# Kernel optimization log

Hardware: AMD Instinct MI355X
Metric: run time of the kernel (lower is better)

Reference implementation:

```python
import jax, jax.numpy as jnp
import numpy as np

NEG_SLOPE = 0.2  # PyG GATConv default leaky_relu slope


def _gat_layer(x, W, att_src, att_dst, bias, src, dst, num_nodes, heads, out_c, concat):
    # x: [N, F_in] -> h: [N, H, C]
    h = (x @ W).reshape(num_nodes, heads, out_c)
    a_src = jnp.einsum('nhc,hc->nh', h, att_src)  # [N, H]
    a_dst = jnp.einsum('nhc,hc->nh', h, att_dst)  # [N, H]
    # edge (src -> dst): attention logit per edge/head
    e = jax.nn.leaky_relu(a_src[src] + a_dst[dst], NEG_SLOPE)  # [E, H]
    # softmax over edges sharing the same destination node
    m = jax.ops.segment_max(e, dst, num_segments=num_nodes)  # [N, H]
    m = jnp.where(jnp.isfinite(m), m, 0.0)
    ex = jnp.exp(e - m[dst])
    denom = jax.ops.segment_sum(ex, dst, num_segments=num_nodes)  # [N, H]
    alpha = ex / (denom[dst] + 1e-16)  # [E, H]
    # weighted scatter-add aggregation
    msg = h[src] * alpha[:, :, None]  # [E, H, C]
    out = jax.ops.segment_sum(msg, dst, num_segments=num_nodes)  # [N, H, C]
    if concat:
        out = out.reshape(num_nodes, heads * out_c)
    else:
        out = out.mean(axis=1)
    return out + bias


def _add_self_loops(edge_index, num_nodes):
    loop = jnp.arange(num_nodes, dtype=edge_index.dtype)
    src = jnp.concatenate([edge_index[0], loop])
    dst = jnp.concatenate([edge_index[1], loop])
    return src, dst


def setup_inputs() -> dict:
    key = jax.random.key(0)
    ks = jax.random.split(key, 9)
    N, F_in, E, H, C, OUT = 30000, 256, 300000, 8, 128, 64
    x = jax.random.normal(ks[0], (N, F_in), dtype=jnp.float32)
    edge_index = jax.random.randint(ks[1], (2, E), 0, N, dtype=jnp.int32)
    s1 = 1.0 / np.sqrt(F_in)
    s2 = 1.0 / np.sqrt(H * C)
    return {
        'x': x,
        'edge_index': edge_index,
        'W1': jax.random.normal(ks[2], (F_in, H * C), dtype=jnp.float32) * s1,
        'att_src1': jax.random.normal(ks[3], (H, C), dtype=jnp.float32) * s2,
        'att_dst1': jax.random.normal(ks[4], (H, C), dtype=jnp.float32) * s2,
        'b1': jnp.zeros((H * C,), dtype=jnp.float32),
        'W2': jax.random.normal(ks[5], (H * C, OUT), dtype=jnp.float32) * s2,
        'att_src2': jax.random.normal(ks[6], (1, OUT), dtype=jnp.float32) * 0.125,
        'att_dst2': jax.random.normal(ks[7], (1, OUT), dtype=jnp.float32) * 0.125,
        'b2': jnp.zeros((OUT,), dtype=jnp.float32),
    }


def reference(x, edge_index, W1, att_src1, att_dst1, b1, W2, att_src2, att_dst2, b2):
    N = x.shape[0]
    src, dst = _add_self_loops(edge_index, N)
    # dropout layers are identity in eval mode
    h = _gat_layer(x, W1, att_src1, att_dst1, b1, src, dst, N, 8, 128, True)
    h = jax.nn.elu(h)
    out = _gat_layer(h, W2, att_src2, att_dst2, b2, src, dst, N, 1, 64, False)
    return jax.nn.log_softmax(out, axis=-1)
```

## Files before the change

### kernel.cpp

```cpp
#include <hip/hip_runtime.h>
#include <math.h>

#define N_NODES 30000
#define F_IN 256
#define E_RAW 300000
#define E_TOT (E_RAW + N_NODES)
#define HEADS 8
#define CH 128
#define HC 1024
#define OUTC 64
#define NEG_SLOPE 0.2f
#define CAP 64

typedef __attribute__((ext_vector_type(8))) short bf16x8;
typedef __attribute__((ext_vector_type(4))) float f32x4;
typedef __attribute__((ext_vector_type(2))) float f32x2;

__device__ __forceinline__ float bf2f(unsigned short u) {
    return __uint_as_float(((unsigned)u) << 16);
}
__device__ __forceinline__ unsigned short f2bf(float f) {
    unsigned b = __float_as_uint(f);
    b += 0x7FFFu + ((b >> 16) & 1u);
    return (unsigned short)(b >> 16);
}
__device__ __forceinline__ void edge_sd(const int* __restrict__ ei, int e, int& s, int& d) {
    if (e < E_RAW) { s = ei[e]; d = ei[E_RAW + e]; }
    else           { s = e - E_RAW; d = s; }
}
__device__ __forceinline__ void async_cp16(const void* g, void* l) {
    __builtin_amdgcn_global_load_lds((const __attribute__((address_space(1))) void*)g,
                                     (__attribute__((address_space(3))) void*)l, 16, 0, 0);
}
__device__ __forceinline__ int slotP(int s) {
    return ((s >> 6) << 6) + ((s >> 2) & 15) + ((s & 3) << 4);
}
__device__ __forceinline__ void wave_sync() {
    __builtin_amdgcn_fence(__ATOMIC_ACQ_REL, "wavefront");
    __builtin_amdgcn_wave_barrier();
}

#define NB_CVTX (N_NODES * F_IN / 4 / 256)
#define NB_DEG  ((E_TOT + 255) / 256)
#define NB_W1T  ((F_IN * HC + 255) / 256)
#define NB_W2T  ((HC * OUTC + 255) / 256)
#define NB_PREP (NB_CVTX + NB_DEG + NB_W1T + NB_W2T)

__global__ __launch_bounds__(256)
void prep_kernel(const float* __restrict__ x, unsigned short* __restrict__ xb,
                 const float* __restrict__ W1, unsigned short* __restrict__ W1t,
                 const float* __restrict__ W2, unsigned short* __restrict__ W2t,
                 const int* __restrict__ ei, int* __restrict__ deg)
{
    const int b = blockIdx.x, t = threadIdx.x;
    if (b < NB_CVTX) {
        int i = b * 256 + t;
        const float4 v = reinterpret_cast<const float4*>(x)[i];
        ushort4 o;
        o.x = f2bf(v.x); o.y = f2bf(v.y); o.z = f2bf(v.z); o.w = f2bf(v.w);
        reinterpret_cast<ushort4*>(xb)[i] = o;
    } else if (b < NB_CVTX + NB_DEG) {
        int e = (b - NB_CVTX) * 256 + t;
        if (e < E_TOT) {
            int s, d; edge_sd(ei, e, s, d);
            atomicAdd(&deg[d], 1);
        }
    } else if (b < NB_CVTX + NB_DEG + NB_W1T) {
        int i = (b - NB_CVTX - NB_DEG) * 256 + t;
        if (i < F_IN * HC) {
            int k = i >> 10, n = i & (HC - 1);
            W1t[n * F_IN + k] = f2bf(W1[i]);
        }
    } else {
        int i = (b - NB_CVTX - NB_DEG - NB_W1T) * 256 + t;
        if (i < HC * OUTC) {
            int s = i >> 6, n = i & (OUTC - 1);
            W2t[n * HC + s] = f2bf(W2[slotP(s) * OUTC + n]);
        }
    }
}

__global__ __launch_bounds__(256)
void gemm1_mfma(const unsigned short* __restrict__ A,
                const unsigned short* __restrict__ Bt,
                unsigned* __restrict__ Cp,
                const float* __restrict__ att_src, const float* __restrict__ att_dst,
                float* __restrict__ a_src, float* __restrict__ a_dst, int M)
{
    __shared__ unsigned short Al[128 * 64];
    __shared__ unsigned short Bl[128 * 64];
    __shared__ float s_src[128][2];
    __shared__ float s_dst[128][2];
    const int tid  = threadIdx.x;
    const int wave = tid >> 6, lane = tid & 63;
    const int quad = lane >> 4, l16 = lane & 15;
    const int wr = (wave >> 1) * 64, wc = (wave & 1) * 64;
    const int row0 = blockIdx.y * 128;
    const int col0 = blockIdx.x * 128;

    f32x4 acc[4][4];
#pragma unroll
    for (int i = 0; i < 4; i++)
#pragma unroll
        for (int j = 0; j < 4; j++) acc[i][j] = (f32x4){0.f, 0.f, 0.f, 0.f};

    for (int k0 = 0; k0 < F_IN; k0 += 64) {
#pragma unroll
        for (int p = 0; p < 4; p++) {
            int idx = tid + 256 * p;
            int r = idx >> 3, q = idx & 7;
            async_cp16(A + (size_t)(row0 + r) * F_IN + k0 + ((q ^ (r & 7)) * 8),
                       Al + (size_t)(wave * 64 + 256 * p) * 8);
        }
#pragma unroll
        for (int p = 0; p < 4; p++) {
            int idx = tid + 256 * p;
            int r = idx >> 3, q = idx & 7;
            async_cp16(Bt + (size_t)(col0 + r) * F_IN + k0 + ((q ^ (r & 7)) * 8),
                       Bl + (size_t)(wave * 64 + 256 * p) * 8);
        }
        __syncthreads();
#pragma unroll
        for (int kh = 0; kh < 2; kh++) {
            const int cx = (kh * 4 + quad) ^ (l16 & 7);
            bf16x8 af[4], bg[4];
#pragma unroll
            for (int i = 0; i < 4; i++)
                af[i] = *reinterpret_cast<const bf16x8*>(Al + ((wr + i * 16 + l16) * 8 + cx) * 8);
#pragma unroll
            for (int j = 0; j < 4; j++)
                bg[j] = *reinterpret_cast<const bf16x8*>(Bl + ((wc + j * 16 + l16) * 8 + cx) * 8);
#pragma unroll
            for (int i = 0; i < 4; i++)
#pragma unroll
                for (int j = 0; j < 4; j++)
                    acc[i][j] = __builtin_amdgcn_mfma_f32_16x16x32_bf16(af[i], bg[j], acc[i][j], 0, 0, 0);
        }
        __syncthreads();
    }
    const int D = ((col0 + wc) >> 6) * 16 + l16;
#pragma unroll
    for (int i = 0; i < 4; i++) {
#pragma unroll
        for (int r = 0; r < 4; r++) {
            int row = row0 + wr + i * 16 + quad * 4 + r;
            if (row >= M) continue;
            int w8 = __builtin_amdgcn_cvt_pk_fp8_f32(acc[i][0][r], acc[i][1][r], 0, false);
            w8 = __builtin_amdgcn_cvt_pk_fp8_f32(acc[i][2][r], acc[i][3][r], w8, true);
            Cp[(size_t)row * 256 + D] = (unsigned)w8;
        }
    }
    const float* asv = att_src + blockIdx.x * CH;
    const float* adv = att_dst + blockIdx.x * CH;
    float av[4], dv[4];
#pragma unroll
    for (int j = 0; j < 4; j++) {
        av[j] = asv[wc + j * 16 + l16];
        dv[j] = adv[wc + j * 16 + l16];
    }
#pragma unroll
    for (int i = 0; i < 4; i++) {
#pragma unroll
        for (int r = 0; r < 4; r++) {
            float ps = 0.f, pd = 0.f;
#pragma unroll
            for (int j = 0; j < 4; j++) {
                float cc = acc[i][j][r];
                ps += cc * av[j];
                pd += cc * dv[j];
            }
#pragma unroll
            for (int o = 1; o < 16; o <<= 1) {
                ps += __shfl_xor(ps, o);
                pd += __shfl_xor(pd, o);
            }
            if (l16 == 0) {
                int lr = wr + i * 16 + quad * 4 + r;
                s_src[lr][wc >> 6] = ps;
                s_dst[lr][wc >> 6] = pd;
            }
        }
    }
    __syncthreads();
    if (tid < 128) {
        int row = row0 + tid;
        if (row < M) {
            a_src[row * 8 + blockIdx.x] = s_src[tid][0] + s_src[tid][1];
            a_dst[row * 8 + blockIdx.x] = s_dst[tid][0] + s_dst[tid][1];
        }
    }
}

__global__ __launch_bounds__(256)
void gemm2_mfma(const unsigned short* __restrict__ A,
                const unsigned short* __restrict__ Bt,
                unsigned short* __restrict__ C,
                const float* __restrict__ att_src2, const float* __restrict__ att_dst2,
                float* __restrict__ a_src2, float* __restrict__ a_dst2, int M)
{
    __shared__ unsigned short Al[64 * 64];
    __shared__ unsigned short Bl[64 * 64];
    const int tid  = threadIdx.x;
    const int wave = tid >> 6, lane = tid & 63;
    const int quad = lane >> 4, l16 = lane & 15;
    const int wr = wave * 16;
    const int row0 = blockIdx.x * 64;

    f32x4 acc[4];
#pragma unroll
    for (int j = 0; j < 4; j++) acc[j] = (f32x4){0.f, 0.f, 0.f, 0.f};

    for (int k0 = 0; k0 < HC; k0 += 64) {
#pragma unroll
        for (int p = 0; p < 2; p++) {
            int idx = tid + 256 * p;
            int r = idx >> 3, q = idx & 7;
            async_cp16(A + (size_t)(row0 + r) * HC + k0 + ((q ^ (r & 7)) * 8),
                       Al + (size_t)(wave * 64 + 256 * p) * 8);
        }
#pragma unroll
        for (int p = 0; p < 2; p++) {
            int idx = tid + 256 * p;
            int r = idx >> 3, q = idx & 7;
            async_cp16(Bt + (size_t)r * HC + k0 + ((q ^ (r & 7)) * 8),
                       Bl + (size_t)(wave * 64 + 256 * p) * 8);
        }
        __syncthreads();
#pragma unroll
        for (int kh = 0; kh < 2; kh++) {
            const int cx = (kh * 4 + quad) ^ (l16 & 7);
            bf16x8 af, bg[4];
            af = *reinterpret_cast<const bf16x8*>(Al + ((wr + l16) * 8 + cx) * 8);
#pragma unroll
            for (int j = 0; j < 4; j++)
                bg[j] = *reinterpret_cast<const bf16x8*>(Bl + ((j * 16 + l16) * 8 + cx) * 8);
#pragma unroll
            for (int j = 0; j < 4; j++)
                acc[j] = __builtin_amdgcn_mfma_f32_16x16x32_bf16(af, bg[j], acc[j], 0, 0, 0);
        }
        __syncthreads();
    }
    float av[4], dv[4];
#pragma unroll
    for (int j = 0; j < 4; j++) {
        av[j] = att_src2[j * 16 + l16];
        dv[j] = att_dst2[j * 16 + l16];
    }
#pragma unroll
    for (int r = 0; r < 4; r++) {
        int row = row0 + wr + quad * 4 + r;
        float ps = 0.f, pd = 0.f;
#pragma unroll
        for (int j = 0; j < 4; j++) {
            float cc = acc[j][r];
            int col = j * 16 + l16;
            if (row < M) C[(size_t)row * OUTC + col] = f2bf(cc);
            ps += cc * av[j];
            pd += cc * dv[j];
        }
#pragma unroll
        for (int o = 1; o < 16; o <<= 1) {
            ps += __shfl_xor(ps, o);
            pd += __shfl_xor(pd, o);
        }
        if (l16 == 0 && row < M) {
            a_src2[row] = ps;
            a_dst2[row] = pd;
        }
    }
}

__global__ __launch_bounds__(256)
void alloc_kernel(const int* __restrict__ deg, int* __restrict__ rowstart,
                  int* __restrict__ cursor, int* __restrict__ counter)
{
    int d = blockIdx.x * 256 + threadIdx.x;
    int lane = threadIdx.x & 63;
    int v = (d < N_NODES) ? deg[d] : 0;
    int x = v;
#pragma unroll
    for (int o = 1; o < 64; o <<= 1) {
        int y = __shfl_up(x, o);
        if (lane >= o) x += y;
    }
    int excl = x - v;
    int total = __shfl(x, 63);
    int base = 0;
    if (lane == 63) base = atomicAdd(counter, total);
    base = __shfl(base, 63);
    if (d < N_NODES) {
        rowstart[d] = base + excl;
        cursor[d]   = base + excl;
    }
}

__global__ void scatter_kernel(const int* __restrict__ ei, int* __restrict__ cursor,
                               int* __restrict__ csr_src)
{
    int e = blockIdx.x * 256 + threadIdx.x;
    if (e >= E_TOT) return;
    int s, d; edge_sd(ei, e, s, d);
    int pos = atomicAdd(&cursor[d], 1);
    csr_src[pos] = s;
}

__global__ __launch_bounds__(256)
void agg1_fused(const int* __restrict__ rowstart, const int* __restrict__ degv,
                const int* __restrict__ csr_src,
                const unsigned* __restrict__ h1p,
                const float* __restrict__ a_src1, const float* __restrict__ a_dst1,
                const float* __restrict__ b1, unsigned short* __restrict__ out1)
{
    const int t   = threadIdx.x;
    const int sub = t >> 6;
    const int tl  = t & 63;
    const int h   = tl >> 3;
    const int d   = blockIdx.x * 4 + sub;

    __shared__ float exps[4][CAP * 8];
    __shared__ int   srcs[4][CAP];

    const int start = rowstart[d];
    const int deg   = degv[d];

    const float adst = a_dst1[d * 8 + h];
    const uint4* __restrict__ h1v = reinterpret_cast<const uint4*>(h1p);

    float denom_part = 0.f;
    float acc[16];
#pragma unroll
    for (int k = 0; k < 16; k++) acc[k] = 0.f;

    for (int c0 = 0; c0 < deg; c0 += CAP) {
        const int cend = min(deg - c0, CAP);
        for (int c = (tl & 7); c < cend; c += 8) {
            int s = csr_src[start + c0 + c];
            if (h == 0) srcs[sub][c] = s;
            float a = a_src1[s * 8 + h] + adst;
            float v = a > 0.f ? a : NEG_SLOPE * a;
            float ex = __expf(v);
            exps[sub][c * 8 + h] = ex;
            denom_part += ex;
        }
        wave_sync();
        {
            int   s_cur = srcs[sub][0];
            float w_cur = exps[sub][h];
            uint4 u_cur = h1v[(size_t)s_cur * 64 + tl];
            for (int c = 0; c < cend; c++) {
                int   s_nxt = 0; float w_nxt = 0.f; uint4 u_nxt;
                if (c + 1 < cend) {
                    s_nxt = srcs[sub][c + 1];
                    w_nxt = exps[sub][(c + 1) * 8 + h];
                    u_nxt = h1v[(size_t)s_nxt * 64 + tl];
                }
#pragma unroll
                for (int dw = 0; dw < 4; dw++) {
                    unsigned wd = (&u_cur.x)[dw];
                    f32x2 lo = __builtin_amdgcn_cvt_pk_f32_fp8((int)wd, false);
                    f32x2 hi = __builtin_amdgcn_cvt_pk_f32_fp8((int)wd, true);
                    acc[dw * 4 + 0] += w_cur * lo.x;
                    acc[dw * 4 + 1] += w_cur * lo.y;
                    acc[dw * 4 + 2] += w_cur * hi.x;
                    acc[dw * 4 + 3] += w_cur * hi.y;
                }
                s_cur = s_nxt; w_cur = w_nxt; u_cur = u_nxt;
            }
        }
        wave_sync();
    }
#pragma unroll
    for (int o = 1; o < 8; o <<= 1) denom_part += __shfl_xor(denom_part, o);
    const float dinv = 1.f / (denom_part + 1e-16f);

    unsigned short ov[16];
#pragma unroll
    for (int e = 0; e < 16; e++) {
        float v = acc[e] * dinv + b1[slotP(16 * tl + e)];
        v = v > 0.f ? v : __expf(v) - 1.f;
        ov[e] = f2bf(v);
    }
    uint4* op = reinterpret_cast<uint4*>(out1 + (size_t)d * HC + 16 * tl);
    op[0] = *reinterpret_cast<uint4*>(&ov[0]);
    op[1] = *reinterpret_cast<uint4*>(&ov[8]);
}

__global__ __launch_bounds__(256)
void agg2_lsm(const int* __restrict__ rowstart, const int* __restrict__ degv,
              const int* __restrict__ csr_src,
              const unsigned short* __restrict__ h2,
              const float* __restrict__ a_src2, const float* __restrict__ a_dst2,
              const float* __restrict__ b2, float* __restrict__ out)
{
    const int t = threadIdx.x;
    const int sub  = t >> 6;
    const int lane = t & 63;
    const int eo   = lane >> 4;
    const int cq   = lane & 15;
    const int d = blockIdx.x * 4 + sub;

    __shared__ float exs[4][CAP];
    __shared__ int   ss[4][CAP];

    const int start = rowstart[d];
    const int deg   = degv[d];

    const float adst = a_dst2[d];
    const uint2* __restrict__ h2v = reinterpret_cast<const uint2*>(h2);
    float denom_part = 0.f;
    float ax = 0.f, ay = 0.f, az = 0.f, aw = 0.f;

    for (int c0 = 0; c0 < deg; c0 += CAP) {
        const int cend = min(deg - c0, CAP);
        for (int c = lane; c < cend; c += 64) {
            int s = csr_src[start + c0 + c];
            ss[sub][c] = s;
            float a = a_src2[s] + adst;
            float v = a > 0.f ? a : NEG_SLOPE * a;
            float ex = __expf(v);
            exs[sub][c] = ex;
            denom_part += ex;
        }
        wave_sync();
        {
            int   cc = eo;
            float w0 = (cc < cend) ? exs[sub][cc] : 0.f;
            int   s0 = (cc < cend) ? ss[sub][cc] : ss[sub][0];
            uint2 u0 = h2v[(size_t)s0 * 16 + cq];
            for (int c = 0; c + 4 < cend; c += 4) {
                int cc1 = c + 4 + eo;
                float w1 = (cc1 < cend) ? exs[sub][cc1] : 0.f;
                int   s1 = (cc1 < cend) ? ss[sub][cc1] : ss[sub][0];
                uint2 u1 = h2v[(size_t)s1 * 16 + cq];
                ax += w0 * __uint_as_float(u0.x << 16);
                ay += w0 * __uint_as_float(u0.x & 0xFFFF0000u);
                az += w0 * __uint_as_float(u0.y << 16);
                aw += w0 * __uint_as_float(u0.y & 0xFFFF0000u);
                w0 = w1; s0 = s1; u0 = u1;
            }
            ax += w0 * __uint_as_float(u0.x << 16);
            ay += w0 * __uint_as_float(u0.x & 0xFFFF0000u);
            az += w0 * __uint_as_float(u0.y << 16);
            aw += w0 * __uint_as_float(u0.y & 0xFFFF0000u);
        }
        wave_sync();
    }
    ax += __shfl_xor(ax, 16); ax += __shfl_xor(ax, 32);
    ay += __shfl_xor(ay, 16); ay += __shfl_xor(ay, 32);
    az += __shfl_xor(az, 16); az += __shfl_xor(az, 32);
    aw += __shfl_xor(aw, 16); aw += __shfl_xor(aw, 32);
#pragma unroll
    for (int o = 32; o > 0; o >>= 1) denom_part += __shfl_xor(denom_part, o);
    const float dinv = 1.f / (denom_part + 1e-16f);

    float4 bb = reinterpret_cast<const float4*>(b2)[cq];
    float v0 = ax * dinv + bb.x;
    float v1 = ay * dinv + bb.y;
    float v2 = az * dinv + bb.z;
    float v3 = aw * dinv + bb.w;
    float m = fmaxf(fmaxf(v0, v1), fmaxf(v2, v3));
#pragma unroll
    for (int o = 1; o < 16; o <<= 1) m = fmaxf(m, __shfl_xor(m, o));
    float ex = __expf(v0 - m) + __expf(v1 - m) + __expf(v2 - m) + __expf(v3 - m);
    float ssum = ex;
#pragma unroll
    for (int o = 1; o < 16; o <<= 1) ssum += __shfl_xor(ssum, o);
    if (eo == 0) {
        float lg = __logf(ssum);
        reinterpret_cast<float4*>(out + (size_t)d * OUTC)[cq] =
            make_float4(v0 - m - lg, v1 - m - lg, v2 - m - lg, v3 - m - lg);
    }
}

extern "C" void kernel_launch(void* const* d_in, const int* in_sizes, int n_in,
                              void* d_out, int out_size, void* d_ws, size_t ws_size,
                              hipStream_t stream)
{
    const float* x   = (const float*)d_in[0];
    const int*   ei  = (const int*)d_in[1];
    const float* W1  = (const float*)d_in[2];
    const float* as1 = (const float*)d_in[3];
    const float* ad1 = (const float*)d_in[4];
    const float* b1  = (const float*)d_in[5];
    const float* W2  = (const float*)d_in[6];
    const float* as2 = (const float*)d_in[7];
    const float* ad2 = (const float*)d_in[8];
    const float* b2  = (const float*)d_in[9];

    char* p = (char*)d_ws;
    auto alloc = [&](size_t bytes) { char* r = p; p += (bytes + 255) & ~(size_t)255; return r; };

    char* region0 = (char*)alloc((size_t)N_NODES * HC * 2);
    unsigned* h1p = (unsigned*)region0;

    char* region1 = (char*)alloc((size_t)N_NODES * HC * 2);
    unsigned short* out1 = (unsigned short*)region1;
    unsigned short* xb   = (unsigned short*)region1;
    unsigned short* W1t  = (unsigned short*)(region1 + (size_t)N_NODES * F_IN * 2 + 256);

    unsigned short* W2t = (unsigned short*)alloc((size_t)OUTC * HC * 2);

    float* a_src1   = (float*)alloc((size_t)N_NODES * HEADS * 4);
    float* a_dst1   = (float*)alloc((size_t)N_NODES * HEADS * 4);
    int*   deg      = (int*)alloc((size_t)(N_NODES + 1) * 4);
    int*   counter  = deg + N_NODES;
    int*   rowstart = (int*)alloc((size_t)N_NODES * 4);
    int*   cursor   = (int*)alloc((size_t)N_NODES * 4);
    int*   csr_src  = (int*)alloc((size_t)E_TOT * 4);

    char* q = region0;
    auto alias = [&](size_t bytes) { char* r = q; q += (bytes + 255) & ~(size_t)255; return r; };
    unsigned short* h2 = (unsigned short*)alias((size_t)N_NODES * OUTC * 2);
    float* a_src2  = (float*)alias((size_t)N_NODES * 4);
    float* a_dst2  = (float*)alias((size_t)N_NODES * 4);

    hipMemsetAsync(deg, 0, (size_t)(N_NODES + 1) * 4, stream);

    prep_kernel<<<NB_PREP, 256, 0, stream>>>(x, xb, W1, W1t, W2, W2t, ei, deg);

    alloc_kernel<<<(N_NODES + 255) / 256, 256, 0, stream>>>(deg, rowstart, cursor, counter);
    scatter_kernel<<<(E_TOT + 255) / 256, 256, 0, stream>>>(ei, cursor, csr_src);

    gemm1_mfma<<<dim3(HC / 128, (N_NODES + 127) / 128), 256, 0, stream>>>(
        xb, W1t, h1p, as1, ad1, a_src1, a_dst1, N_NODES);
    agg1_fused<<<N_NODES / 4, 256, 0, stream>>>(rowstart, deg, csr_src, h1p, a_src1, a_dst1, b1, out1);

    gemm2_mfma<<<(N_NODES + 63) / 64, 256, 0, stream>>>(
        out1, W2t, h2, as2, ad2, a_src2, a_dst2, N_NODES);
    agg2_lsm<<<N_NODES / 4, 256, 0, stream>>>(rowstart, deg, csr_src, h2, a_src2, a_dst2, b2, (float*)d_out);
}
```

Measured before the change: 259.0 us.

## Precompute attention logits via folded W1·att vectors and per-edge exp weights in scatter

Folds att_src/att_dst into W1 (x·(W1·att)) so layer-1 attention logits are computed in fp32 from x during the prep pass, instead of in the GEMM epilogue. The scatter kernel then computes the per-edge exp2 weights (log2e pre-scaled, no max subtraction) and stores them in CSR order, so agg1 no longer gathers a_src or computes exponentials. agg1 also gets a two-deep prefetch and packed FMA accumulation. The costs are an extra small kernel, a 10.5MB per-edge weight buffer, and dropping the softmax max-shift, which assumes the logits stay small.

```diff
diff --git a/kernel.cpp b/kernel.cpp
--- a/kernel.cpp
+++ b/kernel.cpp
@@ -11,14 +11,12 @@
 #define OUTC 64
 #define NEG_SLOPE 0.2f
 #define CAP 64
+#define LOG2E 1.44269504f
 
 typedef __attribute__((ext_vector_type(8))) short bf16x8;
 typedef __attribute__((ext_vector_type(4))) float f32x4;
 typedef __attribute__((ext_vector_type(2))) float f32x2;
 
-__device__ __forceinline__ float bf2f(unsigned short u) {
-    return __uint_as_float(((unsigned)u) << 16);
-}
 __device__ __forceinline__ unsigned short f2bf(float f) {
     unsigned b = __float_as_uint(f);
     b += 0x7FFFu + ((b >> 16) & 1u);
@@ -39,8 +37,32 @@
     __builtin_amdgcn_fence(__ATOMIC_ACQ_REL, "wavefront");
     __builtin_amdgcn_wave_barrier();
 }
-
-#define NB_CVTX (N_NODES * F_IN / 4 / 256)
+__device__ __forceinline__ f32x2 pk_fma(f32x2 a, f32x2 b, f32x2 c) {
+    f32x2 d;
+    asm("v_pk_fma_f32 %0, %1, %2, %3" : "=v"(d) : "v"(a), "v"(b), "v"(c));
+    return d;
+}
+__device__ __forceinline__ float wexp(float t) {
+    return __builtin_amdgcn_exp2f(fmaxf(t, NEG_SLOPE * t));
+}
+
+__global__ __launch_bounds__(256)
+void vsrc_kernel(const float* __restrict__ W1, const float* __restrict__ att_src,
+                 const float* __restrict__ att_dst, float* __restrict__ vsd)
+{
+    const int j = blockIdx.x;
+    const int k = threadIdx.x;
+    const int hj = j & 7;
+    const float* av = (j < 8 ? att_src : att_dst) + hj * CH;
+    const float* wr = W1 + (size_t)k * HC + hj * CH;
+    float s = 0.f;
+#pragma unroll 4
+    for (int c = 0; c < CH; c += 4)
+        s += wr[c] * av[c] + wr[c + 1] * av[c + 1] + wr[c + 2] * av[c + 2] + wr[c + 3] * av[c + 3];
+    vsd[j * 256 + k] = s;
+}
+
+#define NB_CVTX (N_NODES / 16)
 #define NB_DEG  ((E_TOT + 255) / 256)
 #define NB_W1T  ((F_IN * HC + 255) / 256)
 #define NB_W2T  ((HC * OUTC + 255) / 256)
@@ -50,15 +72,40 @@
 void prep_kernel(const float* __restrict__ x, unsigned short* __restrict__ xb,
                  const float* __restrict__ W1, unsigned short* __restrict__ W1t,
                  const float* __restrict__ W2, unsigned short* __restrict__ W2t,
-                 const int* __restrict__ ei, int* __restrict__ deg)
+                 const int* __restrict__ ei, int* __restrict__ deg,
+                 const float* __restrict__ vsd,
+                 float* __restrict__ a_src1, float* __restrict__ a_dst1)
 {
     const int b = blockIdx.x, t = threadIdx.x;
     if (b < NB_CVTX) {
-        int i = b * 256 + t;
-        const float4 v = reinterpret_cast<const float4*>(x)[i];
-        ushort4 o;
-        o.x = f2bf(v.x); o.y = f2bf(v.y); o.z = f2bf(v.z); o.w = f2bf(v.w);
-        reinterpret_cast<ushort4*>(xb)[i] = o;
+        const int w = t >> 6, l = t & 63;
+        const int n0 = b * 16 + w * 4;
+        float4 vs[16];
+        const float4* vs4 = reinterpret_cast<const float4*>(vsd);
+#pragma unroll
+        for (int j = 0; j < 16; j++) vs[j] = vs4[j * 64 + l];
+#pragma unroll 1
+        for (int nn = 0; nn < 4; nn++) {
+            const int n = n0 + nn;
+            const float4 v = reinterpret_cast<const float4*>(x)[(size_t)n * 64 + l];
+            ushort4 o;
+            o.x = f2bf(v.x); o.y = f2bf(v.y); o.z = f2bf(v.z); o.w = f2bf(v.w);
+            reinterpret_cast<ushort4*>(xb)[(size_t)n * 64 + l] = o;
+            float pp[16];
+#pragma unroll
+            for (int j = 0; j < 16; j++)
+                pp[j] = v.x * vs[j].x + v.y * vs[j].y + v.z * vs[j].z + v.w * vs[j].w;
+#pragma unroll
+            for (int o2 = 1; o2 < 64; o2 <<= 1)
+#pragma unroll
+                for (int j = 0; j < 16; j++) pp[j] += __shfl_xor(pp[j], o2);
+            float sel = pp[0];
+#pragma unroll
+            for (int j = 1; j < 16; j++) if (l == j) sel = pp[j];
+            sel *= LOG2E;
+            if (l < 8)       a_src1[n * 8 + l] = sel;
+            else if (l < 16) a_dst1[n * 8 + (l - 8)] = sel;
+        }
     } else if (b < NB_CVTX + NB_DEG) {
         int e = (b - NB_CVTX) * 256 + t;
         if (e < E_TOT) {
@@ -76,196 +123,6 @@
         if (i < HC * OUTC) {
             int s = i >> 6, n = i & (OUTC - 1);
             W2t[n * HC + s] = f2bf(W2[slotP(s) * OUTC + n]);
-        }
-    }
-}
-
-__global__ __launch_bounds__(256)
-void gemm1_mfma(const unsigned short* __restrict__ A,
-                const unsigned short* __restrict__ Bt,
-                unsigned* __restrict__ Cp,
-                const float* __restrict__ att_src, const float* __restrict__ att_dst,
-                float* __restrict__ a_src, float* __restrict__ a_dst, int M)
-{
-    __shared__ unsigned short Al[128 * 64];
-    __shared__ unsigned short Bl[128 * 64];
-    __shared__ float s_src[128][2];
-    __shared__ float s_dst[128][2];
-    const int tid  = threadIdx.x;
-    const int wave = tid >> 6, lane = tid & 63;
-    const int quad = lane >> 4, l16 = lane & 15;
-    const int wr = (wave >> 1) * 64, wc = (wave & 1) * 64;
-    const int row0 = blockIdx.y * 128;
-    const int col0 = blockIdx.x * 128;
-
-    f32x4 acc[4][4];
-#pragma unroll
-    for (int i = 0; i < 4; i++)
-#pragma unroll
-        for (int j = 0; j < 4; j++) acc[i][j] = (f32x4){0.f, 0.f, 0.f, 0.f};
-
-    for (int k0 = 0; k0 < F_IN; k0 += 64) {
-#pragma unroll
-        for (int p = 0; p < 4; p++) {
-            int idx = tid + 256 * p;
-            int r = idx >> 3, q = idx & 7;
-            async_cp16(A + (size_t)(row0 + r) * F_IN + k0 + ((q ^ (r & 7)) * 8),
-                       Al + (size_t)(wave * 64 + 256 * p) * 8);
-        }
-#pragma unroll
-        for (int p = 0; p < 4; p++) {
-            int idx = tid + 256 * p;
-            int r = idx >> 3, q = idx & 7;
-            async_cp16(Bt + (size_t)(col0 + r) * F_IN + k0 + ((q ^ (r & 7)) * 8),
-                       Bl + (size_t)(wave * 64 + 256 * p) * 8);
-        }
-        __syncthreads();
-#pragma unroll
-        for (int kh = 0; kh < 2; kh++) {
-            const int cx = (kh * 4 + quad) ^ (l16 & 7);
-            bf16x8 af[4], bg[4];
-#pragma unroll
-            for (int i = 0; i < 4; i++)
-                af[i] = *reinterpret_cast<const bf16x8*>(Al + ((wr + i * 16 + l16) * 8 + cx) * 8);
-#pragma unroll
-            for (int j = 0; j < 4; j++)
-                bg[j] = *reinterpret_cast<const bf16x8*>(Bl + ((wc + j * 16 + l16) * 8 + cx) * 8);
-#pragma unroll
-            for (int i = 0; i < 4; i++)
-#pragma unroll
-                for (int j = 0; j < 4; j++)
-                    acc[i][j] = __builtin_amdgcn_mfma_f32_16x16x32_bf16(af[i], bg[j], acc[i][j], 0, 0, 0);
-        }
-        __syncthreads();
-    }
-    const int D = ((col0 + wc) >> 6) * 16 + l16;
-#pragma unroll
-    for (int i = 0; i < 4; i++) {
-#pragma unroll
-        for (int r = 0; r < 4; r++) {
-            int row = row0 + wr + i * 16 + quad * 4 + r;
-            if (row >= M) continue;
-            int w8 = __builtin_amdgcn_cvt_pk_fp8_f32(acc[i][0][r], acc[i][1][r], 0, false);
-            w8 = __builtin_amdgcn_cvt_pk_fp8_f32(acc[i][2][r], acc[i][3][r], w8, true);
-            Cp[(size_t)row * 256 + D] = (unsigned)w8;
-        }
-    }
-    const float* asv = att_src + blockIdx.x * CH;
-    const float* adv = att_dst + blockIdx.x * CH;
-    float av[4], dv[4];
-#pragma unroll
-    for (int j = 0; j < 4; j++) {
-        av[j] = asv[wc + j * 16 + l16];
-        dv[j] = adv[wc + j * 16 + l16];
-    }
-#pragma unroll
-    for (int i = 0; i < 4; i++) {
-#pragma unroll
-        for (int r = 0; r < 4; r++) {
-            float ps = 0.f, pd = 0.f;
-#pragma unroll
-            for (int j = 0; j < 4; j++) {
-                float cc = acc[i][j][r];
-                ps += cc * av[j];
-                pd += cc * dv[j];
-            }
-#pragma unroll
-            for (int o = 1; o < 16; o <<= 1) {
-                ps += __shfl_xor(ps, o);
-                pd += __shfl_xor(pd, o);
-            }
-            if (l16 == 0) {
-                int lr = wr + i * 16 + quad * 4 + r;
-                s_src[lr][wc >> 6] = ps;
-                s_dst[lr][wc >> 6] = pd;
-            }
-        }
-    }
-    __syncthreads();
-    if (tid < 128) {
-        int row = row0 + tid;
-        if (row < M) {
-            a_src[row * 8 + blockIdx.x] = s_src[tid][0] + s_src[tid][1];
-            a_dst[row * 8 + blockIdx.x] = s_dst[tid][0] + s_dst[tid][1];
-        }
-    }
-}
-
-__global__ __launch_bounds__(256)
-void gemm2_mfma(const unsigned short* __restrict__ A,
-                const unsigned short* __restrict__ Bt,
-                unsigned short* __restrict__ C,
-                const float* __restrict__ att_src2, const float* __restrict__ att_dst2,
-                float* __restrict__ a_src2, float* __restrict__ a_dst2, int M)
-{
-    __shared__ unsigned short Al[64 * 64];
-    __shared__ unsigned short Bl[64 * 64];
-    const int tid  = threadIdx.x;
-    const int wave = tid >> 6, lane = tid & 63;
-    const int quad = lane >> 4, l16 = lane & 15;
-    const int wr = wave * 16;
-    const int row0 = blockIdx.x * 64;
-
-    f32x4 acc[4];
-#pragma unroll
-    for (int j = 0; j < 4; j++) acc[j] = (f32x4){0.f, 0.f, 0.f, 0.f};
-
-    for (int k0 = 0; k0 < HC; k0 += 64) {
-#pragma unroll
-        for (int p = 0; p < 2; p++) {
-            int idx = tid + 256 * p;
-            int r = idx >> 3, q = idx & 7;
-            async_cp16(A + (size_t)(row0 + r) * HC + k0 + ((q ^ (r & 7)) * 8),
-                       Al + (size_t)(wave * 64 + 256 * p) * 8);
-        }
-#pragma unroll
-        for (int p = 0; p < 2; p++) {
-            int idx = tid + 256 * p;
-            int r = idx >> 3, q = idx & 7;
-            async_cp16(Bt + (size_t)r * HC + k0 + ((q ^ (r & 7)) * 8),
-                       Bl + (size_t)(wave * 64 + 256 * p) * 8);
-        }
-        __syncthreads();
-#pragma unroll
-        for (int kh = 0; kh < 2; kh++) {
-            const int cx = (kh * 4 + quad) ^ (l16 & 7);
-            bf16x8 af, bg[4];
-            af = *reinterpret_cast<const bf16x8*>(Al + ((wr + l16) * 8 + cx) * 8);
-#pragma unroll
-            for (int j = 0; j < 4; j++)
-                bg[j] = *reinterpret_cast<const bf16x8*>(Bl + ((j * 16 + l16) * 8 + cx) * 8);
-#pragma unroll
-            for (int j = 0; j < 4; j++)
-                acc[j] = __builtin_amdgcn_mfma_f32_16x16x32_bf16(af, bg[j], acc[j], 0, 0, 0);
-        }
-        __syncthreads();
-    }
-    float av[4], dv[4];
-#pragma unroll
-    for (int j = 0; j < 4; j++) {
-        av[j] = att_src2[j * 16 + l16];
-        dv[j] = att_dst2[j * 16 + l16];
-    }
-#pragma unroll
-    for (int r = 0; r < 4; r++) {
-        int row = row0 + wr + quad * 4 + r;
-        float ps = 0.f, pd = 0.f;
-#pragma unroll
-        for (int j = 0; j < 4; j++) {
-            float cc = acc[j][r];
-            int col = j * 16 + l16;
-            if (row < M) C[(size_t)row * OUTC + col] = f2bf(cc);
-            ps += cc * av[j];
-            pd += cc * dv[j];
-        }
-#pragma unroll
-        for (int o = 1; o < 16; o <<= 1) {
-            ps += __shfl_xor(ps, o);
-            pd += __shfl_xor(pd, o);
-        }
-        if (l16 == 0 && row < M) {
-            a_src2[row] = ps;
-            a_dst2[row] = pd;
         }
     }
 }
@@ -295,26 +152,110 @@
 }
 
 __global__ void scatter_kernel(const int* __restrict__ ei, int* __restrict__ cursor,
-                               int* __restrict__ csr_src)
+                               int* __restrict__ csr_src,
+                               const float* __restrict__ a_src1,
+                               const float* __restrict__ a_dst1,
+                               float* __restrict__ wcsr)
 {
     int e = blockIdx.x * 256 + threadIdx.x;
     if (e >= E_TOT) return;
     int s, d; edge_sd(ei, e, s, d);
     int pos = atomicAdd(&cursor[d], 1);
     csr_src[pos] = s;
+    const float4* A4 = reinterpret_cast<const float4*>(a_src1);
+    const float4* D4 = reinterpret_cast<const float4*>(a_dst1);
+    float4 sa = A4[s * 2 + 0], sb = A4[s * 2 + 1];
+    float4 da = D4[d * 2 + 0], db = D4[d * 2 + 1];
+    float4 w0, w1;
+    w0.x = wexp(sa.x + da.x); w0.y = wexp(sa.y + da.y);
+    w0.z = wexp(sa.z + da.z); w0.w = wexp(sa.w + da.w);
+    w1.x = wexp(sb.x + db.x); w1.y = wexp(sb.y + db.y);
+    w1.z = wexp(sb.z + db.z); w1.w = wexp(sb.w + db.w);
+    reinterpret_cast<float4*>(wcsr)[pos * 2 + 0] = w0;
+    reinterpret_cast<float4*>(wcsr)[pos * 2 + 1] = w1;
+}
+
+__global__ __launch_bounds__(256)
+void gemm1_mfma(const unsigned short* __restrict__ A,
+                const unsigned short* __restrict__ Bt,
+                unsigned* __restrict__ Cp,
+                int M)
+{
+    __shared__ unsigned short Al[128 * 64];
+    __shared__ unsigned short Bl[128 * 64];
+    const int tid  = threadIdx.x;
+    const int wave = tid >> 6, lane = tid & 63;
+    const int quad = lane >> 4, l16 = lane & 15;
+    const int wr = (wave >> 1) * 64, wc = (wave & 1) * 64;
+    const int row0 = blockIdx.y * 128;
+    const int col0 = blockIdx.x * 128;
+
+    f32x4 acc[4][4];
+#pragma unroll
+    for (int i = 0; i < 4; i++)
+#pragma unroll
+        for (int j = 0; j < 4; j++) acc[i][j] = (f32x4){0.f, 0.f, 0.f, 0.f};
+
+    for (int k0 = 0; k0 < F_IN; k0 += 64) {
+#pragma unroll
+        for (int p = 0; p < 4; p++) {
+            int idx = tid + 256 * p;
+            int r = idx >> 3, q = idx & 7;
+            async_cp16(A + (size_t)(row0 + r) * F_IN + k0 + ((q ^ (r & 7)) * 8),
+                       Al + (size_t)(wave * 64 + 256 * p) * 8);
+        }
+#pragma unroll
+        for (int p = 0; p < 4; p++) {
+            int idx = tid + 256 * p;
+            int r = idx >> 3, q = idx & 7;
+            async_cp16(Bt + (size_t)(col0 + r) * F_IN + k0 + ((q ^ (r & 7)) * 8),
+                       Bl + (size_t)(wave * 64 + 256 * p) * 8);
+        }
+        __syncthreads();
+#pragma unroll
+        for (int kh = 0; kh < 2; kh++) {
+            const int cx = (kh * 4 + quad) ^ (l16 & 7);
+            bf16x8 af[4], bg[4];
+#pragma unroll
+            for (int i = 0; i < 4; i++)
+                af[i] = *reinterpret_cast<const bf16x8*>(Al + ((wr + i * 16 + l16) * 8 + cx) * 8);
+#pragma unroll
+            for (int j = 0; j < 4; j++)
+                bg[j] = *reinterpret_cast<const bf16x8*>(Bl + ((wc + j * 16 + l16) * 8 + cx) * 8);
+#pragma unroll
+            for (int i = 0; i < 4; i++)
+#pragma unroll
+                for (int j = 0; j < 4; j++)
+                    acc[i][j] = __builtin_amdgcn_mfma_f32_16x16x32_bf16(af[i], bg[j], acc[i][j], 0, 0, 0);
+        }
+        __syncthreads();
+    }
+    const int D = ((col0 + wc) >> 6) * 16 + l16;
+#pragma unroll
+    for (int i = 0; i < 4; i++) {
+#pragma unroll
+        for (int r = 0; r < 4; r++) {
+            int row = row0 + wr + i * 16 + quad * 4 + r;
+            if (row >= M) continue;
+            int w8 = __builtin_amdgcn_cvt_pk_fp8_f32(acc[i][0][r], acc[i][1][r], 0, false);
+            w8 = __builtin_amdgcn_cvt_pk_fp8_f32(acc[i][2][r], acc[i][3][r], w8, true);
+            Cp[(size_t)row * 256 + D] = (unsigned)w8;
+        }
+    }
 }
 
 __global__ __launch_bounds__(256)
 void agg1_fused(const int* __restrict__ rowstart, const int* __restrict__ degv,
                 const int* __restrict__ csr_src,
                 const unsigned* __restrict__ h1p,
-                const float* __restrict__ a_src1, const float* __restrict__ a_dst1,
+                const float* __restrict__ wcsr,
                 const float* __restrict__ b1, unsigned short* __restrict__ out1)
 {
     const int t   = threadIdx.x;
     const int sub = t >> 6;
     const int tl  = t & 63;
     const int h   = tl >> 3;
+    const int g   = tl & 7;
     const int d   = blockIdx.x * 4 + sub;
 
     __shared__ float exps[4][CAP * 8];
@@ -322,49 +263,50 @@
 
     const int start = rowstart[d];
     const int deg   = degv[d];
-
-    const float adst = a_dst1[d * 8 + h];
     const uint4* __restrict__ h1v = reinterpret_cast<const uint4*>(h1p);
 
     float denom_part = 0.f;
-    float acc[16];
-#pragma unroll
-    for (int k = 0; k < 16; k++) acc[k] = 0.f;
+    f32x2 acc[8];
+#pragma unroll
+    for (int k = 0; k < 8; k++) acc[k] = (f32x2){0.f, 0.f};
 
     for (int c0 = 0; c0 < deg; c0 += CAP) {
         const int cend = min(deg - c0, CAP);
-        for (int c = (tl & 7); c < cend; c += 8) {
-            int s = csr_src[start + c0 + c];
-            if (h == 0) srcs[sub][c] = s;
-            float a = a_src1[s * 8 + h] + adst;
-            float v = a > 0.f ? a : NEG_SLOPE * a;
-            float ex = __expf(v);
+        for (int c = g; c < cend; c += 8) {
+            int p = start + c0 + c;
+            if (h == 0) srcs[sub][c] = csr_src[p];
+            float ex = wcsr[(size_t)p * 8 + h];
             exps[sub][c * 8 + h] = ex;
             denom_part += ex;
         }
         wave_sync();
         {
-            int   s_cur = srcs[sub][0];
-            float w_cur = exps[sub][h];
-            uint4 u_cur = h1v[(size_t)s_cur * 64 + tl];
+            int   s0 = srcs[sub][0];
+            float w0 = exps[sub][h];
+            uint4 u0 = h1v[(size_t)s0 * 64 + tl];
+            float w1 = 0.f; uint4 u1 = u0;
+            if (1 < cend) {
+                int s1 = srcs[sub][1];
+                w1 = exps[sub][8 + h];
+                u1 = h1v[(size_t)s1 * 64 + tl];
+            }
             for (int c = 0; c < cend; c++) {
-                int   s_nxt = 0; float w_nxt = 0.f; uint4 u_nxt;
-                if (c + 1 < cend) {
-                    s_nxt = srcs[sub][c + 1];
-                    w_nxt = exps[sub][(c + 1) * 8 + h];
-                    u_nxt = h1v[(size_t)s_nxt * 64 + tl];
+                float wn = 0.f; uint4 un = u0;
+                if (c + 2 < cend) {
+                    int sn = srcs[sub][c + 2];
+                    wn = exps[sub][(c + 2) * 8 + h];
+                    un = h1v[(size_t)sn * 64 + tl];
                 }
+                f32x2 w2; w2.x = w0; w2.y = w0;
 #pragma unroll
                 for (int dw = 0; dw < 4; dw++) {
-                    unsigned wd = (&u_cur.x)[dw];
+                    unsigned wd = (&u0.x)[dw];
                     f32x2 lo = __builtin_amdgcn_cvt_pk_f32_fp8((int)wd, false);
                     f32x2 hi = __builtin_amdgcn_cvt_pk_f32_fp8((int)wd, true);
-                    acc[dw * 4 + 0] += w_cur * lo.x;
-                    acc[dw * 4 + 1] += w_cur * lo.y;
-                    acc[dw * 4 + 2] += w_cur * hi.x;
-                    acc[dw * 4 + 3] += w_cur * hi.y;
+                    acc[dw * 2 + 0] = pk_fma(lo, w2, acc[dw * 2 + 0]);
+                    acc[dw * 2 + 1] = pk_fma(hi, w2, acc[dw * 2 + 1]);
                 }
-                s_cur = s_nxt; w_cur = w_nxt; u_cur = u_nxt;
+                w0 = w1; u0 = u1; w1 = wn; u1 = un;
             }
         }
         wave_sync();
@@ -376,13 +318,92 @@
     unsigned short ov[16];
 #pragma unroll
     for (int e = 0; e < 16; e++) {
-        float v = acc[e] * dinv + b1[slotP(16 * tl + e)];
+        float v = ((e & 1) ? acc[e >> 1].y : acc[e >> 1].x) * dinv + b1[slotP(16 * tl + e)];
         v = v > 0.f ? v : __expf(v) - 1.f;
         ov[e] = f2bf(v);
     }
     uint4* op = reinterpret_cast<uint4*>(out1 + (size_t)d * HC + 16 * tl);
     op[0] = *reinterpret_cast<uint4*>(&ov[0]);
     op[1] = *reinterpret_cast<uint4*>(&ov[8]);
+}
+
+__global__ __launch_bounds__(256)
+void gemm2_mfma(const unsigned short* __restrict__ A,
+                const unsigned short* __restrict__ Bt,
+                unsigned short* __restrict__ C,
+                const float* __restrict__ att_src2, const float* __restrict__ att_dst2,
+                float* __restrict__ a_src2, float* __restrict__ a_dst2, int M)
+{
+    __shared__ unsigned short Al[64 * 64];
+    __shared__ unsigned short Bl[64 * 64];
+    const int tid  = threadIdx.x;
+    const int wave = tid >> 6, lane = tid & 63;
+    const int quad = lane >> 4, l16 = lane & 15;
+    const int wr = wave * 16;
+    const int row0 = blockIdx.x * 64;
+
+    f32x4 acc[4];
+#pragma unroll
+    for (int j = 0; j < 4; j++) acc[j] = (f32x4){0.f, 0.f, 0.f, 0.f};
+
+    for (int k0 = 0; k0 < HC; k0 += 64) {
+#pragma unroll
+        for (int p = 0; p < 2; p++) {
+            int idx = tid + 256 * p;
+            int r = idx >> 3, q = idx & 7;
+            async_cp16(A + (size_t)(row0 + r) * HC + k0 + ((q ^ (r & 7)) * 8),
+                       Al + (size_t)(wave * 64 + 256 * p) * 8);
+        }
+#pragma unroll
+        for (int p = 0; p < 2; p++) {
+            int idx = tid + 256 * p;
+            int r = idx >> 3, q = idx & 7;
+            async_cp16(Bt + (size_t)r * HC + k0 + ((q ^ (r & 7)) * 8),
+                       Bl + (size_t)(wave * 64 + 256 * p) * 8);
+        }
+        __syncthreads();
+#pragma unroll
+        for (int kh = 0; kh < 2; kh++) {
+            const int cx = (kh * 4 + quad) ^ (l16 & 7);
+            bf16x8 af, bg[4];
+            af = *reinterpret_cast<const bf16x8*>(Al + ((wr + l16) * 8 + cx) * 8);
+#pragma unroll
+            for (int j = 0; j < 4; j++)
+                bg[j] = *reinterpret_cast<const bf16x8*>(Bl + ((j * 16 + l16) * 8 + cx) * 8);
+#pragma unroll
+            for (int j = 0; j < 4; j++)
+                acc[j] = __builtin_amdgcn_mfma_f32_16x16x32_bf16(af, bg[j], acc[j], 0, 0, 0);
+        }
+        __syncthreads();
+    }
+    float av[4], dv[4];
+#pragma unroll
+    for (int j = 0; j < 4; j++) {
+        av[j] = att_src2[j * 16 + l16];
+        dv[j] = att_dst2[j * 16 + l16];
+    }
+#pragma unroll
+    for (int r = 0; r < 4; r++) {
+        int row = row0 + wr + quad * 4 + r;
+        float ps = 0.f, pd = 0.f;
+#pragma unroll
+        for (int j = 0; j < 4; j++) {
+            float cc = acc[j][r];
+            int col = j * 16 + l16;
+            if (row < M) C[(size_t)row * OUTC + col] = f2bf(cc);
+            ps += cc * av[j];
+            pd += cc * dv[j];
+        }
+#pragma unroll
+        for (int o = 1; o < 16; o <<= 1) {
+            ps += __shfl_xor(ps, o);
+            pd += __shfl_xor(pd, o);
+        }
+        if (l16 == 0 && row < M) {
+            a_src2[row] = ps;
+            a_dst2[row] = pd;
+        }
+    }
 }
 
 __global__ __launch_bounds__(256)
@@ -499,6 +520,8 @@
     unsigned short* W1t  = (unsigned short*)(region1 + (size_t)N_NODES * F_IN * 2 + 256);
 
     unsigned short* W2t = (unsigned short*)alloc((size_t)OUTC * HC * 2);
+    float* vsd = (float*)alloc(16 * 256 * 4);
+    float* wcsr = (float*)alloc((size_t)E_TOT * 8 * 4);
 
     float* a_src1   = (float*)alloc((size_t)N_NODES * HEADS * 4);
     float* a_dst1   = (float*)alloc((size_t)N_NODES * HEADS * 4);
@@ -516,14 +539,18 @@
 
     hipMemsetAsync(deg, 0, (size_t)(N_NODES + 1) * 4, stream);
 
-    prep_kernel<<<NB_PREP, 256, 0, stream>>>(x, xb, W1, W1t, W2, W2t, ei, deg);
+    vsrc_kernel<<<16, 256, 0, stream>>>(W1, as1, ad1, vsd);
+
+    prep_kernel<<<NB_PREP, 256, 0, stream>>>(x, xb, W1, W1t, W2, W2t, ei, deg,
+                                             vsd, a_src1, a_dst1);
 
     alloc_kernel<<<(N_NODES + 255) / 256, 256, 0, stream>>>(deg, rowstart, cursor, counter);
-    scatter_kernel<<<(E_TOT + 255) / 256, 256, 0, stream>>>(ei, cursor, csr_src);
+    scatter_kernel<<<(E_TOT + 255) / 256, 256, 0, stream>>>(ei, cursor, csr_src,
+                                                            a_src1, a_dst1, wcsr);
 
     gemm1_mfma<<<dim3(HC / 128, (N_NODES + 127) / 128), 256, 0, stream>>>(
-        xb, W1t, h1p, as1, ad1, a_src1, a_dst1, N_NODES);
-    agg1_fused<<<N_NODES / 4, 256, 0, stream>>>(rowstart, deg, csr_src, h1p, a_src1, a_dst1, b1, out1);
+        xb, W1t, h1p, N_NODES);
+    agg1_fused<<<N_NODES / 4, 256, 0, stream>>>(rowstart, deg, csr_src, h1p, wcsr, b1, out1);
 
     gemm2_mfma<<<(N_NODES + 63) / 64, 256, 0, stream>>>(
         out1, W2t, h2, as2, ad2, a_src2, a_dst2, N_NODES);
```

New measurement: 272.0 us. 1.05x slower.
